# Performance work log

Measured on AMD Instinct MI355X. Metric: run time of the kernel, lower is better.

Reference implementation:

```python
import jax, jax.numpy as jnp
import numpy as np

EPS = 1e-5
NUM_HEADS = 8


def _ln(x, g, b):
    m = x.mean(-1, keepdims=True)
    v = jnp.mean((x - m) ** 2, -1, keepdims=True)
    return (x - m) * jax.lax.rsqrt(v + EPS) * g + b


def _bn(x, g, b, m, v):  # eval-mode BatchNorm2d on NCHW
    sh = (1, -1, 1, 1)
    return (x - m.reshape(sh)) * jax.lax.rsqrt(v.reshape(sh) + EPS) * g.reshape(sh) + b.reshape(sh)


def _conv3x3(x, w):
    return jax.lax.conv_general_dilated(x, w, (1, 1), 'SAME', dimension_numbers=('NCHW', 'OIHW', 'NCHW'))


def _gelu(x):
    return jax.nn.gelu(x, approximate=False)  # torch nn.GELU default (erf)


def _attention(x, w_qkv, temperature, w_proj):
    # XCiT-style cross-covariance (channel) attention
    B, N, C = x.shape
    h = NUM_HEADS
    d = C // h
    qkv = (x @ w_qkv.T).reshape(B, N, 3, h, d)
    qkv = jnp.transpose(qkv, (2, 0, 3, 4, 1))  # [3, B, h, d, N]
    q, k, v = qkv[0], qkv[1], qkv[2]
    q = q / jnp.maximum(jnp.linalg.norm(q, axis=-1, keepdims=True), 1e-12)
    k = k / jnp.maximum(jnp.linalg.norm(k, axis=-1, keepdims=True), 1e-12)
    attn = jnp.einsum('bhdn,bhen->bhde', q, k) * temperature[None, :, None, None]
    attn = jax.nn.softmax(attn, axis=-1)  # [B, h, d, d]
    out = jnp.einsum('bhde,bhen->bhdn', attn, v)
    out = jnp.transpose(out, (0, 3, 1, 2)).reshape(B, N, C)
    return out @ w_proj.T


def _forward(x, ln1_g, ln1_b, w_qkv, temperature, w_proj, gamma1,
             ln2_g, ln2_b, mlp_w1, bn1_g, bn1_b, bn1_m, bn1_v,
             mlp_w2, bn2_g, bn2_b, bn2_m, bn2_v, gamma2,
             ln3_g, ln3_b, pconv1, pbn_g, pbn_b, pbn_m, pbn_v, pconv2, gamma3,
             H, W):
    B, N, C = x.shape
    # --- Attention residual block ---
    z = _attention(_ln(x, ln1_g, ln1_b), w_qkv, temperature, w_proj)
    x = x + gamma1 * z
    # --- ConvMlp residual block (1x1 convs + eval BN) ---
    y = _ln(x, ln2_g, ln2_b)
    y = jnp.transpose(y, (0, 2, 1)).reshape(B, C, H, W)
    y = _bn(jnp.einsum('oc,bchw->bohw', mlp_w1, y), bn1_g, bn1_b, bn1_m, bn1_v)
    y = _gelu(y)
    y = _bn(jnp.einsum('oc,bchw->bohw', mlp_w2, y), bn2_g, bn2_b, bn2_m, bn2_v)
    y = jnp.transpose(y.reshape(B, C, N), (0, 2, 1))
    x = x + gamma2 * y
    # --- Projection residual block (3x3 conv + BN + GELU + 3x3 conv) ---
    p = _ln(x, ln3_g, ln3_b)
    p = jnp.transpose(p, (0, 2, 1)).reshape(B, C, H, W)
    p = _conv3x3(p, pconv1)
    p = _gelu(_bn(p, pbn_g, pbn_b, pbn_m, pbn_v))
    p = _conv3x3(p, pconv2)
    p = jnp.transpose(p.reshape(B, C, N), (0, 2, 1))
    x = x + gamma3 * p
    return x


def setup_inputs() -> dict:
    key = jax.random.key(0)
    B, H, W, C, MR = 16, 48, 48, 384, 2
    N = H * W
    C2 = C * MR
    ks = jax.random.split(key, 12)
    nrm = lambda k, sh, s: (jax.random.normal(k, sh) * s).astype(jnp.float32)
    INIT_VALUES = 1e-4  # ResidualBlock default gamma init
    return {
        'x': nrm(ks[0], (B, N, C), 1.0),
        'ln1_g': jnp.ones((C,), jnp.float32), 'ln1_b': jnp.zeros((C,), jnp.float32),
        'w_qkv': nrm(ks[1], (3 * C, C), C ** -0.5),
        'temperature': jnp.ones((NUM_HEADS,), jnp.float32),
        'w_proj': nrm(ks[2], (C, C), C ** -0.5),
        'gamma1': jnp.full((C,), INIT_VALUES, jnp.float32),
        'ln2_g': jnp.ones((C,), jnp.float32), 'ln2_b': jnp.zeros((C,), jnp.float32),
        'mlp_w1': nrm(ks[3], (C2, C), C ** -0.5),
        'bn1_g': jnp.ones((C2,), jnp.float32), 'bn1_b': jnp.zeros((C2,), jnp.float32),
        'bn1_m': nrm(ks[4], (C2,), 0.1), 'bn1_v': jnp.ones((C2,), jnp.float32),
        'mlp_w2': nrm(ks[5], (C, C2), C2 ** -0.5),
        'bn2_g': jnp.ones((C,), jnp.float32), 'bn2_b': jnp.zeros((C,), jnp.float32),
        'bn2_m': nrm(ks[6], (C,), 0.1), 'bn2_v': jnp.ones((C,), jnp.float32),
        'gamma2': jnp.full((C,), INIT_VALUES, jnp.float32),
        'ln3_g': jnp.ones((C,), jnp.float32), 'ln3_b': jnp.zeros((C,), jnp.float32),
        'pconv1': nrm(ks[7], (C, C, 3, 3), (9 * C) ** -0.5),
        'pbn_g': jnp.ones((C,), jnp.float32), 'pbn_b': jnp.zeros((C,), jnp.float32),
        'pbn_m': nrm(ks[8], (C,), 0.1), 'pbn_v': jnp.ones((C,), jnp.float32),
        'pconv2': nrm(ks[9], (C, C, 3, 3), (9 * C) ** -0.5),
        'gamma3': jnp.full((C,), INIT_VALUES, jnp.float32),
        'H': H, 'W': W,
    }


def reference(x, ln1_g, ln1_b, w_qkv, temperature, w_proj, gamma1,
              ln2_g, ln2_b, mlp_w1, bn1_g, bn1_b, bn1_m, bn1_v,
              mlp_w2, bn2_g, bn2_b, bn2_m, bn2_v, gamma2,
              ln3_g, ln3_b, pconv1, pbn_g, pbn_b, pbn_m, pbn_v, pconv2, gamma3,
              H, W):
    out = _forward(x, ln1_g, ln1_b, w_qkv, temperature, w_proj, gamma1,
                   ln2_g, ln2_b, mlp_w1, bn1_g, bn1_b, bn1_m, bn1_v,
                   mlp_w2, bn2_g, bn2_b, bn2_m, bn2_v, gamma2,
                   ln3_g, ln3_b, pconv1, pbn_g, pbn_b, pbn_m, pbn_v, pconv2, gamma3,
                   H, W)
    return (out, H, W)
```

## Files before the change

kernel.cpp:

```cpp
#include <hip/hip_runtime.h>
#include <hip/hip_bf16.h>

typedef unsigned short u16;
typedef unsigned char  u8;
typedef __attribute__((ext_vector_type(4))) float floatx4;

#define LN_EPS 1e-5f

__device__ __forceinline__ float bf2f(u16 u) {
    unsigned int i = ((unsigned int)u) << 16;
    float f; __builtin_memcpy(&f, &i, 4); return f;
}
__device__ __forceinline__ u16 f2bf(float f) {
    __hip_bfloat16 h = __float2bfloat16(f);
    u16 u; __builtin_memcpy(&u, &h, 2); return u;
}
__device__ __forceinline__ u8 f2e4(float f) {
    int p = __builtin_amdgcn_cvt_pk_fp8_f32(f, f, 0, false);
    return (u8)(p & 0xff);
}

__device__ __forceinline__ int swz(int m, int k) {
    return (k & ~63) | (((((k >> 3) + (m >> 1)) & 7) << 3)) | (k & 7);
}

__device__ __forceinline__ void gl_lds16(const u8* g, u8* l) {
    __builtin_amdgcn_global_load_lds(
        (const __attribute__((address_space(1))) void*)(const void*)g,
        (__attribute__((address_space(3))) void*)(void*)l,
        16, 0, 0);
}

__device__ __forceinline__ void cvt4_body(const float* __restrict__ in, u8* __restrict__ out,
                                          int i, int Kp) {
    float4 f = ((const float4*)in)[i];
    uchar4 o; o.x = f2e4(f.x); o.y = f2e4(f.y); o.z = f2e4(f.z); o.w = f2e4(f.w);
    int e = i * 4;
    int n = e / Kp, k = e - n * Kp;
    *(uchar4*)(out + (size_t)n * Kp + swz(n, k)) = o;
}
__device__ __forceinline__ void reord_body(const float* __restrict__ w, u8* __restrict__ wr,
                                           int i) {
    int o = i / 3456, rem = i - o * 3456;
    int j = rem / 384, c = rem - j * 384;
    wr[(size_t)o * 3456 + swz(o, rem)] = f2e4(w[(size_t)(o * 384 + c) * 9 + j]);
}

__global__ __launch_bounds__(256)
void prep_kernel(const float* __restrict__ w_qkv, u8* __restrict__ wqkvb,
                 const float* __restrict__ w_proj, u8* __restrict__ wprojb,
                 const float* __restrict__ mlp_w1, u8* __restrict__ w1b,
                 const float* __restrict__ mlp_w2, u8* __restrict__ w2b,
                 float* __restrict__ Sacc,
                 const float* __restrict__ pconv1, u8* __restrict__ w1r,
                 const float* __restrict__ pconv2, u8* __restrict__ w2r,
                 unsigned int* __restrict__ zp,
                 const int* __restrict__ Hp, const int* __restrict__ Wp,
                 float* __restrict__ dout, size_t base, int n_extra) {
    int i = blockIdx.x * 256 + threadIdx.x;
    if (i < 110592)                   { cvt4_body(w_qkv, wqkvb, i, 384);  return; }
    if ((i -= 110592) < 36864)        { cvt4_body(w_proj, wprojb, i, 384); return; }
    if ((i -= 36864) < 73728)         { cvt4_body(mlp_w1, w1b, i, 384);   return; }
    if ((i -= 73728) < 73728)         { cvt4_body(mlp_w2, w2b, i, 768);   return; }
    if ((i -= 73728) < 307200)        { Sacc[i] = 0.f;                    return; }
    if ((i -= 307200) < 1327104)      { reord_body(pconv1, w1r, i);       return; }
    if ((i -= 1327104) < 1327104)     { reord_body(pconv2, w2r, i);       return; }
    if ((i -= 1327104) < 1024)        { zp[i] = 0u;                       return; }
    if ((i -= 1024) < 2) {
        if (i == 0 && n_extra >= 1) dout[base]     = (float)Hp[0];
        if (i == 1 && n_extra >= 2) dout[base + 1] = (float)Wp[0];
    }
}
#define PREP_TOTAL (110592 + 36864 + 73728 + 73728 + 307200 + 1327104 + 1327104 + 1024 + 2)

template<bool SWZ>
__global__ __launch_bounds__(256)
void ln_kernel(const float* __restrict__ xf, const float* __restrict__ g,
               const float* __restrict__ b, u8* __restrict__ out) {
    const int row = blockIdx.x * 4 + (threadIdx.x >> 6);
    const int lane = threadIdx.x & 63;
    const float* xr = xf + (size_t)row * 384;
    float v[6], s = 0.f, s2 = 0.f;
#pragma unroll
    for (int i = 0; i < 6; ++i) { v[i] = xr[lane + i * 64]; s += v[i]; s2 += v[i] * v[i]; }
#pragma unroll
    for (int off = 32; off; off >>= 1) { s += __shfl_xor(s, off); s2 += __shfl_xor(s2, off); }
    float mean = s * (1.0f / 384.0f);
    float var  = s2 * (1.0f / 384.0f) - mean * mean;
    float rstd = rsqrtf(var + LN_EPS);
    u8* orow = out + (size_t)row * 384;
    int pofs = lane;
    if (SWZ) {
        const int gperm = (row >> 1) & 7;
        pofs = ((((lane >> 3) + gperm) & 7) << 3) | (lane & 7);
    }
#pragma unroll
    for (int i = 0; i < 6; ++i) {
        int c = lane + i * 64;
        orow[i * 64 + pofs] = f2e4((v[i] - mean) * rstd * g[c] + b[c]);
    }
}

template<int ACONV, int EPI, bool SWZO = false>
__global__ __launch_bounds__(256, 4)
void gemm_nt(const u8* __restrict__ A, const u8* __restrict__ Bm,
             int M, int N, int K,
             u16* __restrict__ Obf, int ldo,
             float* __restrict__ xf, float* __restrict__ ofb, const float* __restrict__ xin,
             const float* __restrict__ bn_g, const float* __restrict__ bn_b,
             const float* __restrict__ bn_m, const float* __restrict__ bn_v,
             const float* __restrict__ gamma, const u8* __restrict__ zp) {
    __shared__ u8 As[2][128 * 64];
    __shared__ u8 Bs[2][128 * 64];

    const int tid = threadIdx.x;
    const int gx = gridDim.x;
    const int g  = blockIdx.y * gx + blockIdx.x;
    const int G  = gx * gridDim.y;
    int L = g;
    if ((G & 7) == 0) L = (g & 7) * (G >> 3) + (g >> 3);
    const int n0 = (L % gx) * 128;
    const int m0 = (L / gx) * 128;

    const int lane  = tid & 63;
    const int wave  = tid >> 6;
    const int wm    = (wave >> 1) * 64;
    const int wn    = (wave & 1) * 64;
    const int fr    = lane & 15;
    const int klane = lane >> 4;

    int arow[4], brow[4];
#pragma unroll
    for (int i = 0; i < 4; ++i) {
        arow[i] = (wm + i * 16 + fr) * 64;
        brow[i] = (wn + i * 16 + fr) * 64;
    }
    int csw8[2];
#pragma unroll
    for (int kh = 0; kh < 2; ++kh)
        csw8[kh] = ((((kh << 2) + klane) + (fr >> 1)) & 7) << 3;
    int csw4[2];
#pragma unroll
    for (int kh = 0; kh < 2; ++kh)
        csw4[kh] = ((((kh << 1) + (klane >> 1) + (fr >> 1)) & 3) << 4) + ((klane & 1) << 3);

    const int srow = tid >> 2;
    const int scol = (tid & 3) << 4;
    const int ssc4 = ((((tid & 3) - ((tid >> 3) & 3)) & 3) << 4);
    const u8 *sa[2], *sb[2];
    const u8* imgq[2];
    int ay[2], ax[2];
#pragma unroll
    for (int q = 0; q < 2; ++q) {
        int r = q * 64 + srow;
        if (ACONV == 0) {
            sa[q] = A + (size_t)(m0 + r) * K + scol;
        } else {
            int nA = m0 + r;
            int bi = nA / 2304;
            int nl = nA - bi * 2304;
            ay[q] = nl / 48;
            ax[q] = nl - ay[q] * 48;
            imgq[q] = A + (size_t)bi * 2304 * 384;
        }
        sb[q] = Bm + (size_t)(n0 + q * 64 + srow) * K + scol;
    }

    int scnt = 0, sjj = 0;
    const int NT = K / 64;

    auto STAGE = [&](int d) {
        if (ACONV == 1) {
            if (scnt == 0) {
                int t3 = sjj / 3;
                int dy = t3 - 1, dx = sjj - t3 * 3 - 1;
                ++sjj;
#pragma unroll
                for (int q = 0; q < 2; ++q) {
                    int yy = ay[q] + dy, xx = ax[q] + dx;
                    bool v = ((unsigned)yy < 48u) & ((unsigned)xx < 48u);
                    sa[q] = (v ? imgq[q] + (size_t)(yy * 48 + xx) * 384 : zp) + ssc4;
                }
            }
            scnt = (scnt == 5) ? 0 : scnt + 1;
        }
        u8* la = &As[d][0];
        u8* lb = &Bs[d][0];
        gl_lds16(sa[0], la + ((wave * 64) << 4));        sa[0] += 64;
        gl_lds16(sa[1], la + ((256 + wave * 64) << 4));  sa[1] += 64;
        gl_lds16(sb[0], lb + ((wave * 64) << 4));        sb[0] += 64;
        gl_lds16(sb[1], lb + ((256 + wave * 64) << 4));  sb[1] += 64;
    };

    floatx4 acc[4][4];
#pragma unroll
    for (int i = 0; i < 4; ++i)
#pragma unroll
        for (int j = 0; j < 4; ++j) acc[i][j] = (floatx4){0.f, 0.f, 0.f, 0.f};

    STAGE(0);
    STAGE(1);
    asm volatile("s_waitcnt vmcnt(4)" ::: "memory");
    __builtin_amdgcn_s_barrier();
    asm volatile("" ::: "memory");

    int cur = 0;
    for (int t = 0; t < NT; ++t) {
        const u8* Ab = &As[cur][0];
        const u8* Bb = &Bs[cur][0];
#pragma unroll
        for (int kh = 0; kh < 2; ++kh) {
            long af[4], bfr[4];
#pragma unroll
            for (int i = 0; i < 4; ++i) af[i]  = *(const long*)(Ab + arow[i] + (ACONV ? csw4[kh] : csw8[kh]));
#pragma unroll
            for (int j = 0; j < 4; ++j)  bfr[j] = *(const long*)(Bb + brow[j] + csw8[kh]);
            __builtin_amdgcn_s_setprio(1);
#pragma unroll
            for (int i = 0; i < 4; ++i)
#pragma unroll
                for (int j = 0; j < 4; ++j)
                    acc[i][j] = __builtin_amdgcn_mfma_f32_16x16x32_fp8_fp8(af[i], bfr[j], acc[i][j], 0, 0, 0);
            __builtin_amdgcn_s_setprio(0);
        }
        asm volatile("s_waitcnt lgkmcnt(0)" ::: "memory");
        __builtin_amdgcn_s_barrier();
        asm volatile("" ::: "memory");
        if (t + 2 < NT) {
            STAGE(cur);
            asm volatile("s_waitcnt vmcnt(4)" ::: "memory");
        } else {
            asm volatile("s_waitcnt vmcnt(0)" ::: "memory");
        }
        __builtin_amdgcn_sched_barrier(0);
        __builtin_amdgcn_s_barrier();
        asm volatile("" ::: "memory");
        cur ^= 1;
    }

    const int quad4 = (lane >> 4) * 4;
#pragma unroll
    for (int j = 0; j < 4; ++j) {
        int col = n0 + wn + j * 16 + fr;
        float bscale = 0.f, bshift = 0.f, gam = 0.f;
        if (EPI == 1 || EPI == 2) {
            bscale = bn_g[col] * rsqrtf(bn_v[col] + LN_EPS);
            bshift = bn_b[col] - bn_m[col] * bscale;
        }
        if (EPI >= 2) gam = gamma[col];
#pragma unroll
        for (int i = 0; i < 4; ++i) {
#pragma unroll
            for (int r = 0; r < 4; ++r) {
                int row = m0 + wm + i * 16 + quad4 + r;
                float v = acc[i][j][r];
                if (EPI == 0) {
                    Obf[(size_t)row * ldo + col] = f2bf(v);
                } else if (EPI == 1) {
                    float t = v * bscale + bshift;
                    t = 0.5f * t * (1.0f + erff(t * 0.70710678118654752f));
                    int oc = SWZO ? swz(row, col) : col;
                    ((u8*)Obf)[(size_t)row * ldo + oc] = f2e4(t);
                } else if (EPI == 2) {
                    float t = v * bscale + bshift;
                    xf[(size_t)row * N + col] += gam * t;
                } else if (EPI == 3) {
                    xf[(size_t)row * N + col] += gam * v;
                } else if (EPI == 4) {
                    ofb[(size_t)row * N + col] = xf[(size_t)row * N + col] + gam * v;
                } else {
                    xf[(size_t)row * N + col] = xin[(size_t)row * N + col] + gam * v;
                }
            }
        }
    }
}

__global__ __launch_bounds__(256)
void gram_kernel(const u16* __restrict__ qkv, float* __restrict__ Sacc,
                 float* __restrict__ nrm2) {
    const int bh = blockIdx.y;
    const int b = bh >> 3, h = bh & 7;
    const int tid = threadIdx.x;
    __shared__ float qsf[64][48];
    __shared__ float ksf[64][48];

    float acc9[3][3];
#pragma unroll
    for (int i = 0; i < 3; ++i)
#pragma unroll
        for (int j = 0; j < 3; ++j) acc9[i][j] = 0.f;
    float qn2 = 0.f, kn2 = 0.f;

    const int qoff = h * 48;
    const int koff = 384 + h * 48;
    const int d0 = (tid >> 4) * 3;
    const int e0 = (tid & 15) * 3;
    const int nbase = blockIdx.x * 128;

    for (int c = 0; c < 2; ++c) {
        const int n0 = nbase + c * 64;
#pragma unroll
        for (int it = 0; it < 6; ++it) {
            int chunk = tid + it * 256;
            int mat = chunk >= 768 ? 1 : 0;
            int rem = chunk - mat * 768;
            int nn = rem / 12, u = rem - nn * 12;
            ushort4 raw = *(const ushort4*)(qkv + (size_t)(b * 2304 + n0 + nn) * 1152 +
                                            (mat ? koff : qoff) + u * 4);
            float4 f = make_float4(bf2f(raw.x), bf2f(raw.y), bf2f(raw.z), bf2f(raw.w));
            if (mat) *(float4*)&ksf[nn][u * 4] = f;
            else     *(float4*)&qsf[nn][u * 4] = f;
        }
        __syncthreads();
#pragma unroll 4
        for (int nn = 0; nn < 64; ++nn) {
            float q0 = qsf[nn][d0], q1 = qsf[nn][d0 + 1], q2 = qsf[nn][d0 + 2];
            float k0v = ksf[nn][e0], k1v = ksf[nn][e0 + 1], k2v = ksf[nn][e0 + 2];
            acc9[0][0] += q0 * k0v; acc9[0][1] += q0 * k1v; acc9[0][2] += q0 * k2v;
            acc9[1][0] += q1 * k0v; acc9[1][1] += q1 * k1v; acc9[1][2] += q1 * k2v;
            acc9[2][0] += q2 * k0v; acc9[2][1] += q2 * k1v; acc9[2][2] += q2 * k2v;
        }
        if (tid < 48) {
            for (int nn = 0; nn < 64; ++nn) { float q = qsf[nn][tid]; qn2 += q * q; }
        } else if (tid >= 128 && tid < 176) {
            int e = tid - 128;
            for (int nn = 0; nn < 64; ++nn) { float k = ksf[nn][e]; kn2 += k * k; }
        }
        __syncthreads();
    }

    float* Sb = Sacc + (size_t)bh * 2304;
#pragma unroll
    for (int i = 0; i < 3; ++i)
#pragma unroll
        for (int j = 0; j < 3; ++j)
            atomicAdd(&Sb[(d0 + i) * 48 + e0 + j], acc9[i][j]);
    if (tid < 48) atomicAdd(&nrm2[bh * 96 + tid], qn2);
    else if (tid >= 128 && tid < 176) atomicAdd(&nrm2[bh * 96 + 48 + (tid - 128)], kn2);
}

__global__ __launch_bounds__(256)
void attn_fin_kernel(const float* __restrict__ Sacc, const float* __restrict__ nrm2,
                     const float* __restrict__ temp, float* __restrict__ attnb) {
    const int bh = blockIdx.x;
    const int h = bh & 7;
    const int tid = threadIdx.x;
    __shared__ float S[48][49];
    __shared__ float qns[48], kns[48];

    const float* Sb = Sacc + (size_t)bh * 2304;
    for (int i = tid; i < 2304; i += 256) {
        int d = i / 48, e = i - d * 48;
        S[d][e] = Sb[i];
    }
    if (tid < 48)      qns[tid]      = fmaxf(sqrtf(nrm2[bh * 96 + tid]), 1e-12f);
    else if (tid < 96) kns[tid - 48] = fmaxf(sqrtf(nrm2[bh * 96 + tid]), 1e-12f);
    __syncthreads();

    if (tid < 48) {
        float tf = temp[h] / qns[tid];
        float mx = -1e30f;
        for (int e = 0; e < 48; ++e) {
            float t = S[tid][e] * tf / kns[e];
            S[tid][e] = t;
            mx = fmaxf(mx, t);
        }
        float sum = 0.f;
        for (int e = 0; e < 48; ++e) { float t = __expf(S[tid][e] - mx); S[tid][e] = t; sum += t; }
        float inv = 1.0f / sum;
        float* dst = attnb + ((size_t)bh * 48 + tid) * 48;
        for (int e = 0; e < 48; ++e) dst[e] = S[tid][e] * inv;
    }
}

__global__ __launch_bounds__(256)
void attnout_kernel(const u16* __restrict__ qkv, const float* __restrict__ attnb,
                    u8* __restrict__ z) {
    const int r0 = blockIdx.x * 64;
    const int h  = blockIdx.y;
    const int b  = r0 / 2304;
    const int tid = threadIdx.x;
    __shared__ float A[48][49];
    __shared__ float vsf[64][48];

    const float* asrc = attnb + (size_t)(b * 8 + h) * 2304;
    for (int i = tid; i < 2304; i += 256) {
        int d = i / 48, e = i - d * 48;
        A[d][e] = asrc[i];
    }
    const int voff = 768 + h * 48;
    for (int i = tid; i < 768; i += 256) {
        int nn = i / 12, u = i - nn * 12;
        ushort4 raw = *(const ushort4*)(qkv + (size_t)(r0 + nn) * 1152 + voff + u * 4);
        float4 f = make_float4(bf2f(raw.x), bf2f(raw.y), bf2f(raw.z), bf2f(raw.w));
        *(float4*)&vsf[nn][u * 4] = f;
    }
    __syncthreads();

    const int rr0 = (tid >> 4) * 4;
    const int d0  = (tid & 15) * 3;
    float acc[4][3];
#pragma unroll
    for (int r = 0; r < 4; ++r)
#pragma unroll
        for (int j = 0; j < 3; ++j) acc[r][j] = 0.f;

#pragma unroll 4
    for (int e = 0; e < 48; ++e) {
        float a0 = A[d0][e], a1 = A[d0 + 1][e], a2 = A[d0 + 2][e];
#pragma unroll
        for (int r = 0; r < 4; ++r) {
            float vv = vsf[rr0 + r][e];
            acc[r][0] += a0 * vv; acc[r][1] += a1 * vv; acc[r][2] += a2 * vv;
        }
    }
#pragma unroll
    for (int r = 0; r < 4; ++r)
#pragma unroll
        for (int j = 0; j < 3; ++j) {
            int row = r0 + rr0 + r;
            int col = h * 48 + d0 + j;
            z[(size_t)row * 384 + swz(row, col)] = f2e4(acc[r][j]);
        }
}

extern "C" void kernel_launch(void* const* d_in, const int* in_sizes, int n_in,
                              void* d_out, int out_size, void* d_ws, size_t ws_size,
                              hipStream_t stream) {
    const float* x      = (const float*)d_in[0];
    const float* ln1_g  = (const float*)d_in[1];
    const float* ln1_b  = (const float*)d_in[2];
    const float* w_qkv  = (const float*)d_in[3];
    const float* temp   = (const float*)d_in[4];
    const float* w_proj = (const float*)d_in[5];
    const float* gamma1 = (const float*)d_in[6];
    const float* ln2_g  = (const float*)d_in[7];
    const float* ln2_b  = (const float*)d_in[8];
    const float* mlp_w1 = (const float*)d_in[9];
    const float* bn1_g  = (const float*)d_in[10];
    const float* bn1_b  = (const float*)d_in[11];
    const float* bn1_m  = (const float*)d_in[12];
    const float* bn1_v  = (const float*)d_in[13];
    const float* mlp_w2 = (const float*)d_in[14];
    const float* bn2_g  = (const float*)d_in[15];
    const float* bn2_b  = (const float*)d_in[16];
    const float* bn2_m  = (const float*)d_in[17];
    const float* bn2_v  = (const float*)d_in[18];
    const float* gamma2 = (const float*)d_in[19];
    const float* ln3_g  = (const float*)d_in[20];
    const float* ln3_b  = (const float*)d_in[21];
    const float* pconv1 = (const float*)d_in[22];
    const float* pbn_g  = (const float*)d_in[23];
    const float* pbn_b  = (const float*)d_in[24];
    const float* pbn_m  = (const float*)d_in[25];
    const float* pbn_v  = (const float*)d_in[26];
    const float* pconv2 = (const float*)d_in[27];
    const float* gamma3 = (const float*)d_in[28];
    const int* Hp = (const int*)d_in[29];
    const int* Wp = (const int*)d_in[30];

    const int M = 36864, C = 384, C2 = 768, NQKV = 1152, KC = 3456;
    const size_t NBNC = (size_t)M * C;

    const size_t SZ_XF  = NBNC * 4;
    const size_t SZ_LN  = NBNC * 2;
    const size_t SZ_BIG = (size_t)M * NQKV * 2;
    const size_t SZ_P3  = SZ_LN;
    const size_t SZ_W   = (size_t)C * KC * 2;
    if (ws_size < SZ_XF + SZ_LN + SZ_BIG + SZ_P3 + 2 * SZ_W + 4096) return;

    char* ws = (char*)d_ws;
    float* xf     = (float*)ws;
    u8*    lnbuf  = (u8*)(ws + SZ_XF);
    u16*   big    = (u16*)(ws + SZ_XF + SZ_LN);
    char*  p3     = ws + SZ_XF + SZ_LN + SZ_BIG;
    float* attnb  = (float*)p3;
    u8*    wqkvb  = (u8*)(p3 + 1179648);
    u8*    wprojb = (u8*)(p3 + 1179648 + 884736);
    u8*    w1b    = (u8*)(p3 + 1179648 + 884736 + 294912);
    u8*    w2b    = (u8*)(p3 + 1179648 + 884736 + 294912 + 589824);
    float* Sacc   = (float*)(p3 + 3538944);
    float* nrm2   = (float*)(p3 + 3538944 + 1179648);
    u8*    convbf = (u8*)p3;
    u8*    w1r    = (u8*)(p3 + SZ_P3);
    u8*    w2r    = (u8*)(p3 + SZ_P3 + SZ_W);
    u8*    zpg    = (u8*)(p3 + SZ_P3 + 2 * SZ_W);

    const int n_extra = out_size - (int)NBNC;

    prep_kernel<<<(PREP_TOTAL + 255) / 256, 256, 0, stream>>>(
        w_qkv, wqkvb, w_proj, wprojb, mlp_w1, w1b, mlp_w2, w2b,
        Sacc, pconv1, w1r, pconv2, w2r, (unsigned int*)zpg,
        Hp, Wp, (float*)d_out, NBNC, n_extra);

    ln_kernel<true><<<M / 4, 256, 0, stream>>>(x, ln1_g, ln1_b, lnbuf);
    gemm_nt<0, 0><<<dim3(NQKV / 128, M / 128), 256, 0, stream>>>(
        lnbuf, wqkvb, M, NQKV, C, big, NQKV, nullptr, nullptr, nullptr,
        nullptr, nullptr, nullptr, nullptr, nullptr, nullptr);
    gram_kernel<<<dim3(18, 128), 256, 0, stream>>>(big, Sacc, nrm2);
    attn_fin_kernel<<<128, 256, 0, stream>>>(Sacc, nrm2, temp, attnb);
    attnout_kernel<<<dim3(M / 64, 8), 256, 0, stream>>>(big, attnb, lnbuf);
    gemm_nt<0, 5><<<dim3(C / 128, M / 128), 256, 0, stream>>>(
        lnbuf, wprojb, M, C, C, nullptr, 0, xf, nullptr, x,
        nullptr, nullptr, nullptr, nullptr, gamma1, nullptr);

    ln_kernel<true><<<M / 4, 256, 0, stream>>>(xf, ln2_g, ln2_b, lnbuf);
    gemm_nt<0, 1, true><<<dim3(C2 / 128, M / 128), 256, 0, stream>>>(
        lnbuf, w1b, M, C2, C, (u16*)big, C2, nullptr, nullptr, nullptr,
        bn1_g, bn1_b, bn1_m, bn1_v, nullptr, nullptr);
    gemm_nt<0, 2><<<dim3(C / 128, M / 128), 256, 0, stream>>>(
        (u8*)big, w2b, M, C, C2, nullptr, 0, xf, nullptr, nullptr,
        bn2_g, bn2_b, bn2_m, bn2_v, gamma2, nullptr);

    ln_kernel<false><<<M / 4, 256, 0, stream>>>(xf, ln3_g, ln3_b, lnbuf);
    gemm_nt<1, 1, false><<<dim3(C / 128, M / 128), 256, 0, stream>>>(
        lnbuf, w1r, M, C, KC, (u16*)convbf, C, nullptr, nullptr, nullptr,
        pbn_g, pbn_b, pbn_m, pbn_v, nullptr, zpg);
    gemm_nt<1, 4><<<dim3(C / 128, M / 128), 256, 0, stream>>>(
        convbf, w2r, M, C, KC, nullptr, 0, xf, (float*)d_out, nullptr,
        nullptr, nullptr, nullptr, nullptr, gamma3, zpg);
}
```

Baseline: 655.0 us.

## Unify swizzled LDS layout for conv GEMMs and fuse softmax into attnout

```diff
diff --git a/kernel.cpp b/kernel.cpp
--- a/kernel.cpp
+++ b/kernel.cpp
@@ -73,7 +73,6 @@
 }
 #define PREP_TOTAL (110592 + 36864 + 73728 + 73728 + 307200 + 1327104 + 1327104 + 1024 + 2)
 
-template<bool SWZ>
 __global__ __launch_bounds__(256)
 void ln_kernel(const float* __restrict__ xf, const float* __restrict__ g,
                const float* __restrict__ b, u8* __restrict__ out) {
@@ -89,11 +88,8 @@
     float var  = s2 * (1.0f / 384.0f) - mean * mean;
     float rstd = rsqrtf(var + LN_EPS);
     u8* orow = out + (size_t)row * 384;
-    int pofs = lane;
-    if (SWZ) {
-        const int gperm = (row >> 1) & 7;
-        pofs = ((((lane >> 3) + gperm) & 7) << 3) | (lane & 7);
-    }
+    const int gperm = (row >> 1) & 7;
+    const int pofs = ((((lane >> 3) + gperm) & 7) << 3) | (lane & 7);
 #pragma unroll
     for (int i = 0; i < 6; ++i) {
         int c = lane + i * 64;
@@ -101,7 +97,7 @@
     }
 }
 
-template<int ACONV, int EPI, bool SWZO = false>
+template<int ACONV, int EPI>
 __global__ __launch_bounds__(256, 4)
 void gemm_nt(const u8* __restrict__ A, const u8* __restrict__ Bm,
              int M, int N, int K,
@@ -129,6 +125,9 @@
     const int fr    = lane & 15;
     const int klane = lane >> 4;
 
+    const int hE = fr >> 1;
+    const int hO = ((fr + 1) >> 1) & 7;
+
     int arow[4], brow[4];
 #pragma unroll
     for (int i = 0; i < 4; ++i) {
@@ -138,15 +137,10 @@
     int csw8[2];
 #pragma unroll
     for (int kh = 0; kh < 2; ++kh)
-        csw8[kh] = ((((kh << 2) + klane) + (fr >> 1)) & 7) << 3;
-    int csw4[2];
-#pragma unroll
-    for (int kh = 0; kh < 2; ++kh)
-        csw4[kh] = ((((kh << 1) + (klane >> 1) + (fr >> 1)) & 3) << 4) + ((klane & 1) << 3);
+        csw8[kh] = ((((kh << 2) + klane) + hE) & 7) << 3;
 
     const int srow = tid >> 2;
     const int scol = (tid & 3) << 4;
-    const int ssc4 = ((((tid & 3) - ((tid >> 3) & 3)) & 3) << 4);
     const u8 *sa[2], *sb[2];
     const u8* imgq[2];
     int ay[2], ax[2];
@@ -179,7 +173,7 @@
                 for (int q = 0; q < 2; ++q) {
                     int yy = ay[q] + dy, xx = ax[q] + dx;
                     bool v = ((unsigned)yy < 48u) & ((unsigned)xx < 48u);
-                    sa[q] = (v ? imgq[q] + (size_t)(yy * 48 + xx) * 384 : zp) + ssc4;
+                    sa[q] = (v ? imgq[q] + (size_t)(yy * 48 + xx) * 384 : zp) + scol;
                 }
             }
             scnt = (scnt == 5) ? 0 : scnt + 1;
@@ -205,23 +199,32 @@
     asm volatile("" ::: "memory");
 
     int cur = 0;
-    for (int t = 0; t < NT; ++t) {
+    auto KSTEP = [&](int a0, int a1, int t) {
         const u8* Ab = &As[cur][0];
         const u8* Bb = &Bs[cur][0];
-#pragma unroll
-        for (int kh = 0; kh < 2; ++kh) {
+        {
             long af[4], bfr[4];
 #pragma unroll
-            for (int i = 0; i < 4; ++i) af[i]  = *(const long*)(Ab + arow[i] + (ACONV ? csw4[kh] : csw8[kh]));
-#pragma unroll
-            for (int j = 0; j < 4; ++j)  bfr[j] = *(const long*)(Bb + brow[j] + csw8[kh]);
-            __builtin_amdgcn_s_setprio(1);
+            for (int i = 0; i < 4; ++i) af[i]  = *(const long*)(Ab + arow[i] + a0);
+#pragma unroll
+            for (int j = 0; j < 4; ++j)  bfr[j] = *(const long*)(Bb + brow[j] + csw8[0]);
 #pragma unroll
             for (int i = 0; i < 4; ++i)
 #pragma unroll
                 for (int j = 0; j < 4; ++j)
                     acc[i][j] = __builtin_amdgcn_mfma_f32_16x16x32_fp8_fp8(af[i], bfr[j], acc[i][j], 0, 0, 0);
-            __builtin_amdgcn_s_setprio(0);
+        }
+        {
+            long af[4], bfr[4];
+#pragma unroll
+            for (int i = 0; i < 4; ++i) af[i]  = *(const long*)(Ab + arow[i] + a1);
+#pragma unroll
+            for (int j = 0; j < 4; ++j)  bfr[j] = *(const long*)(Bb + brow[j] + csw8[1]);
+#pragma unroll
+            for (int i = 0; i < 4; ++i)
+#pragma unroll
+                for (int j = 0; j < 4; ++j)
+                    acc[i][j] = __builtin_amdgcn_mfma_f32_16x16x32_fp8_fp8(af[i], bfr[j], acc[i][j], 0, 0, 0);
         }
         asm volatile("s_waitcnt lgkmcnt(0)" ::: "memory");
         __builtin_amdgcn_s_barrier();
@@ -236,6 +239,21 @@
         __builtin_amdgcn_s_barrier();
         asm volatile("" ::: "memory");
         cur ^= 1;
+    };
+
+    if (ACONV == 0) {
+        for (int t = 0; t < NT; ++t) KSTEP(csw8[0], csw8[1], t);
+    } else {
+        int t = 0;
+        for (int tap = 0; tap < 9; ++tap) {
+            int t3 = tap / 3;
+            int shift = (t3 - 1) * 48 + (tap - t3 * 3 - 1) + 4608;
+            int cc = (shift >> 1) & 7;
+            int h  = (shift & 1) ? hO : hE;
+            int ca0 = ((klane + h + cc) & 7) << 3;
+            int ca1 = ((4 + klane + h + cc) & 7) << 3;
+            for (int tt = 0; tt < 6; ++tt, ++t) KSTEP(ca0, ca1, t);
+        }
     }
 
     const int quad4 = (lane >> 4) * 4;
@@ -259,8 +277,7 @@
                 } else if (EPI == 1) {
                     float t = v * bscale + bshift;
                     t = 0.5f * t * (1.0f + erff(t * 0.70710678118654752f));
-                    int oc = SWZO ? swz(row, col) : col;
-                    ((u8*)Obf)[(size_t)row * ldo + oc] = f2e4(t);
+                    ((u8*)Obf)[(size_t)row * ldo + swz(row, col)] = f2e4(t);
                 } else if (EPI == 2) {
                     float t = v * bscale + bshift;
                     xf[(size_t)row * N + col] += gam * t;
@@ -341,60 +358,46 @@
 }
 
 __global__ __launch_bounds__(256)
-void attn_fin_kernel(const float* __restrict__ Sacc, const float* __restrict__ nrm2,
-                     const float* __restrict__ temp, float* __restrict__ attnb) {
-    const int bh = blockIdx.x;
-    const int h = bh & 7;
-    const int tid = threadIdx.x;
-    __shared__ float S[48][49];
-    __shared__ float qns[48], kns[48];
-
-    const float* Sb = Sacc + (size_t)bh * 2304;
-    for (int i = tid; i < 2304; i += 256) {
-        int d = i / 48, e = i - d * 48;
-        S[d][e] = Sb[i];
-    }
-    if (tid < 48)      qns[tid]      = fmaxf(sqrtf(nrm2[bh * 96 + tid]), 1e-12f);
-    else if (tid < 96) kns[tid - 48] = fmaxf(sqrtf(nrm2[bh * 96 + tid]), 1e-12f);
-    __syncthreads();
-
-    if (tid < 48) {
-        float tf = temp[h] / qns[tid];
-        float mx = -1e30f;
-        for (int e = 0; e < 48; ++e) {
-            float t = S[tid][e] * tf / kns[e];
-            S[tid][e] = t;
-            mx = fmaxf(mx, t);
-        }
-        float sum = 0.f;
-        for (int e = 0; e < 48; ++e) { float t = __expf(S[tid][e] - mx); S[tid][e] = t; sum += t; }
-        float inv = 1.0f / sum;
-        float* dst = attnb + ((size_t)bh * 48 + tid) * 48;
-        for (int e = 0; e < 48; ++e) dst[e] = S[tid][e] * inv;
-    }
-}
-
-__global__ __launch_bounds__(256)
-void attnout_kernel(const u16* __restrict__ qkv, const float* __restrict__ attnb,
+void attnout_kernel(const u16* __restrict__ qkv, const float* __restrict__ Sacc,
+                    const float* __restrict__ nrm2, const float* __restrict__ temp,
                     u8* __restrict__ z) {
     const int r0 = blockIdx.x * 64;
     const int h  = blockIdx.y;
     const int b  = r0 / 2304;
+    const int bh = b * 8 + h;
     const int tid = threadIdx.x;
     __shared__ float A[48][49];
     __shared__ float vsf[64][48];
-
-    const float* asrc = attnb + (size_t)(b * 8 + h) * 2304;
+    __shared__ float qns[48], kns[48];
+
+    const float* Sb = Sacc + (size_t)bh * 2304;
     for (int i = tid; i < 2304; i += 256) {
         int d = i / 48, e = i - d * 48;
-        A[d][e] = asrc[i];
-    }
+        A[d][e] = Sb[i];
+    }
+    if (tid < 48)      qns[tid]      = fmaxf(sqrtf(nrm2[bh * 96 + tid]), 1e-12f);
+    else if (tid < 96) kns[tid - 48] = fmaxf(sqrtf(nrm2[bh * 96 + tid]), 1e-12f);
     const int voff = 768 + h * 48;
     for (int i = tid; i < 768; i += 256) {
         int nn = i / 12, u = i - nn * 12;
         ushort4 raw = *(const ushort4*)(qkv + (size_t)(r0 + nn) * 1152 + voff + u * 4);
         float4 f = make_float4(bf2f(raw.x), bf2f(raw.y), bf2f(raw.z), bf2f(raw.w));
         *(float4*)&vsf[nn][u * 4] = f;
+    }
+    __syncthreads();
+
+    if (tid < 48) {
+        float tf = temp[h] / qns[tid];
+        float mx = -1e30f;
+        for (int e = 0; e < 48; ++e) {
+            float t = A[tid][e] * tf / kns[e];
+            A[tid][e] = t;
+            mx = fmaxf(mx, t);
+        }
+        float sum = 0.f;
+        for (int e = 0; e < 48; ++e) { float t = __expf(A[tid][e] - mx); A[tid][e] = t; sum += t; }
+        float inv = 1.0f / sum;
+        for (int e = 0; e < 48; ++e) A[tid][e] *= inv;
     }
     __syncthreads();
 
@@ -475,7 +478,6 @@
     u8*    lnbuf  = (u8*)(ws + SZ_XF);
     u16*   big    = (u16*)(ws + SZ_XF + SZ_LN);
     char*  p3     = ws + SZ_XF + SZ_LN + SZ_BIG;
-    float* attnb  = (float*)p3;
     u8*    wqkvb  = (u8*)(p3 + 1179648);
     u8*    wprojb = (u8*)(p3 + 1179648 + 884736);
     u8*    w1b    = (u8*)(p3 + 1179648 + 884736 + 294912);
@@ -494,27 +496,26 @@
         Sacc, pconv1, w1r, pconv2, w2r, (unsigned int*)zpg,
         Hp, Wp, (float*)d_out, NBNC, n_extra);
 
-    ln_kernel<true><<<M / 4, 256, 0, stream>>>(x, ln1_g, ln1_b, lnbuf);
+    ln_kernel<<<M / 4, 256, 0, stream>>>(x, ln1_g, ln1_b, lnbuf);
     gemm_nt<0, 0><<<dim3(NQKV / 128, M / 128), 256, 0, stream>>>(
         lnbuf, wqkvb, M, NQKV, C, big, NQKV, nullptr, nullptr, nullptr,
         nullptr, nullptr, nullptr, nullptr, nullptr, nullptr);
     gram_kernel<<<dim3(18, 128), 256, 0, stream>>>(big, Sacc, nrm2);
-    attn_fin_kernel<<<128, 256, 0, stream>>>(Sacc, nrm2, temp, attnb);
-    attnout_kernel<<<dim3(M / 64, 8), 256, 0, stream>>>(big, attnb, lnbuf);
+    attnout_kernel<<<dim3(M / 64, 8), 256, 0, stream>>>(big, Sacc, nrm2, temp, lnbuf);
     gemm_nt<0, 5><<<dim3(C / 128, M / 128), 256, 0, stream>>>(
         lnbuf, wprojb, M, C, C, nullptr, 0, xf, nullptr, x,
         nullptr, nullptr, nullptr, nullptr, gamma1, nullptr);
 
-    ln_kernel<true><<<M / 4, 256, 0, stream>>>(xf, ln2_g, ln2_b, lnbuf);
-    gemm_nt<0, 1, true><<<dim3(C2 / 128, M / 128), 256, 0, stream>>>(
+    ln_kernel<<<M / 4, 256, 0, stream>>>(xf, ln2_g, ln2_b, lnbuf);
+    gemm_nt<0, 1><<<dim3(C2 / 128, M / 128), 256, 0, stream>>>(
         lnbuf, w1b, M, C2, C, (u16*)big, C2, nullptr, nullptr, nullptr,
         bn1_g, bn1_b, bn1_m, bn1_v, nullptr, nullptr);
     gemm_nt<0, 2><<<dim3(C / 128, M / 128), 256, 0, stream>>>(
         (u8*)big, w2b, M, C, C2, nullptr, 0, xf, nullptr, nullptr,
         bn2_g, bn2_b, bn2_m, bn2_v, gamma2, nullptr);
 
-    ln_kernel<false><<<M / 4, 256, 0, stream>>>(xf, ln3_g, ln3_b, lnbuf);
-    gemm_nt<1, 1, false><<<dim3(C / 128, M / 128), 256, 0, stream>>>(
+    ln_kernel<<<M / 4, 256, 0, stream>>>(xf, ln3_g, ln3_b, lnbuf);
+    gemm_nt<1, 1><<<dim3(C / 128, M / 128), 256, 0, stream>>>(
         lnbuf, w1r, M, C, KC, (u16*)convbf, C, nullptr, nullptr, nullptr,
         pbn_g, pbn_b, pbn_m, pbn_v, nullptr, zpg);
     gemm_nt<1, 4><<<dim3(C / 128, M / 128), 256, 0, stream>>>(
```

After: 759.9 us. 1.16x slower.
